# Optimization experiments

Hardware: AMD Instinct MI355X
Metric: run time of the kernel (lower is better)

The kernel has to match this reference:

```python
import jax, jax.numpy as jnp
import numpy as np

S = 3072       # packed sequence length
DIM = 1280     # hidden dim
H = 16         # num heads
HD = DIM // H  # head dim = 80
NEG = -1e9     # additive mask value for cross-segment entries


def setup_inputs() -> dict:
    key = jax.random.key(0)
    ks = jax.random.split(key, 6)
    x = jax.random.normal(ks[0], (S, DIM), jnp.float32)
    # rope angle table [S, HD//2]
    rotary_pos_emb = jax.random.uniform(ks[1], (S, HD // 2), jnp.float32, 0.0, 2.0 * np.pi)
    # 4 equal image segments packed together
    cu_seqlens = jnp.array([0, 768, 1536, 2304, 3072], jnp.int32)
    w_qkv = jax.random.normal(ks[2], (3 * DIM, DIM), jnp.float32) * 0.02
    b_qkv = jax.random.normal(ks[3], (3 * DIM,), jnp.float32) * 0.02
    w_proj = jax.random.normal(ks[4], (DIM, DIM), jnp.float32) * 0.02
    b_proj = jax.random.normal(ks[5], (DIM,), jnp.float32) * 0.02
    return {"x": x, "cu_seqlens": cu_seqlens, "rotary_pos_emb": rotary_pos_emb,
            "w_qkv": w_qkv, "b_qkv": b_qkv, "w_proj": w_proj, "b_proj": b_proj}


def _rope(t, cos, sin):
    # t: [S, H, HD]; cos/sin: [S, 1, HD]
    t1, t2 = jnp.split(t, 2, axis=-1)
    rot = jnp.concatenate([-t2, t1], axis=-1)
    return t * cos + rot * sin


def reference(x, cu_seqlens, rotary_pos_emb, w_qkv, b_qkv, w_proj, b_proj):
    s, d = x.shape
    qkv = (x @ w_qkv.T + b_qkv).reshape(s, 3, H, HD)
    q, k, v = qkv[:, 0], qkv[:, 1], qkv[:, 2]  # each [S, H, HD]

    # NeoX-style rope with tiled (repeated) freqs, computed in fp32
    cos = jnp.cos(rotary_pos_emb)
    sin = jnp.sin(rotary_pos_emb)
    cos = jnp.concatenate([cos, cos], axis=-1)[:, None, :]  # [S,1,HD]
    sin = jnp.concatenate([sin, sin], axis=-1)[:, None, :]
    q = _rope(q.astype(jnp.float32), cos, sin).astype(x.dtype)
    k = _rope(k.astype(jnp.float32), cos, sin).astype(x.dtype)

    # block-diagonal varlen mask from cu_seqlens: segment id per position
    seg = jnp.searchsorted(cu_seqlens, jnp.arange(s), side='right') - 1  # [S]
    mask = jnp.where(seg[:, None] == seg[None, :], 0.0, NEG).astype(x.dtype)  # [S,S]

    scale = 1.0 / np.sqrt(HD).astype(np.float32)
    scores = jnp.einsum('qhd,khd->hqk', q, k) * scale + mask[None]  # [H,S,S]
    attn = jax.nn.softmax(scores, axis=-1)
    out = jnp.einsum('hqk,khd->qhd', attn, v).reshape(s, d)  # [S, DIM]
    return out @ w_proj.T + b_proj
```

## Files before the change

### kernel.cpp

```cpp
#include <hip/hip_runtime.h>


typedef __bf16 bf16;
typedef __bf16 bf16x4 __attribute__((ext_vector_type(4)));
typedef __bf16 bf16x8 __attribute__((ext_vector_type(8)));
typedef float f32x4 __attribute__((ext_vector_type(4)));
typedef float f32x16 __attribute__((ext_vector_type(16)));
typedef unsigned int u32;

constexpr int S = 3072;
constexpr int DIM = 1280;
constexpr int H = 16;
constexpr int HD = 80;
constexpr int KDP = 128;
constexpr int NQKV = 3 * DIM;

constexpr int BM = 192;
constexpr int MB_A = S / BM;
constexpr int NB_B = NQKV / 256;
constexpr int NKT = DIM / 32;
constexpr int ASL = BM * 32 * 2;
constexpr int SLOT = ASL + 16384;

constexpr float QSCALE = 1.4426950408889634f / 8.94427190999916f;

__device__ __forceinline__ void gload_lds16(const void* g, void* l) {
  __builtin_amdgcn_global_load_lds(
      (const __attribute__((address_space(1))) void*)g,
      (__attribute__((address_space(3))) void*)l, 16, 0, 0);
}

__device__ __forceinline__ u32 pkbf2(float a, float b) {
  union { bf16 h[2]; u32 w; } u;
  u.h[0] = (bf16)a; u.h[1] = (bf16)b;
  return u.w;
}

__device__ __forceinline__ int swv(int s) {
  return ((((s >> 3) & 31) ^ ((s & 7) << 2)) << 2);
}

constexpr long PA_CHUNKS = (long)MB_A * NKT * (ASL / 16);
constexpr long PB_CHUNKS = (long)NB_B * NKT * 1024;
constexpr long PW_CHUNKS = (long)DIM * DIM / 8;
constexpr long KP_CHUNKS = (long)H * S * 48 / 8;
constexpr long CS_CHUNKS = (long)S * 40 / 8;
constexpr long TOT_CHUNKS = PA_CHUNKS + PB_CHUNKS + PW_CHUNKS + KP_CHUNKS + CS_CHUNKS;

__global__ __launch_bounds__(256) void pack_inputs(
    const float* __restrict__ x, const float* __restrict__ wq,
    const float* __restrict__ wp, const float* __restrict__ rope,
    bf16* __restrict__ pA, bf16* __restrict__ pB, bf16* __restrict__ wp16,
    bf16* __restrict__ Kb, float* __restrict__ ctab, float* __restrict__ stab) {
  long t = (long)blockIdx.x * 256 + threadIdx.x;
  if (t < PA_CHUNKS) {
    const int blk = (int)(t / (NKT * 768)), rem = (int)(t % (NKT * 768));
    const int kt = rem / 768, c = rem - kt * 768;
    const int lin = c * 16;
    const int logi = lin ^ (((lin >> 7) & 7) << 4);
    const int row = logi >> 6, col = (logi & 63) >> 1;
    const float* src = x + (size_t)(blk * BM + row) * DIM + kt * 32 + col;
    float4 v0 = *(const float4*)src;
    float4 v1 = *(const float4*)(src + 4);
    bf16x8 o = {(bf16)v0.x, (bf16)v0.y, (bf16)v0.z, (bf16)v0.w,
                (bf16)v1.x, (bf16)v1.y, (bf16)v1.z, (bf16)v1.w};
    *(bf16x8*)(pA + t * 8) = o;
  } else if (t < PA_CHUNKS + PB_CHUNKS) {
    long t2 = t - PA_CHUNKS;
    const int blk = (int)(t2 / (NKT * 1024)), rem = (int)(t2 % (NKT * 1024));
    const int kt = rem >> 10, c = rem & 1023;
    const int lin = c * 16;
    const int logi = lin ^ (((lin >> 7) & 7) << 4);
    const int row = logi >> 6, col = (logi & 63) >> 1;
    int grow = blk * 256 + row;
    if (grow < 2560) {
      const int ty = grow / 1280, rm = grow % 1280;
      const int h = rm / 80, p = rm % 80;
      grow = ty * 1280 + h * 80 + (p >> 1) + (p & 1) * 40;
    }
    const float* src = wq + (size_t)grow * DIM + kt * 32 + col;
    float4 v0 = *(const float4*)src;
    float4 v1 = *(const float4*)(src + 4);
    bf16x8 o = {(bf16)v0.x, (bf16)v0.y, (bf16)v0.z, (bf16)v0.w,
                (bf16)v1.x, (bf16)v1.y, (bf16)v1.z, (bf16)v1.w};
    *(bf16x8*)(pB + t2 * 8) = o;
  } else if (t < PA_CHUNKS + PB_CHUNKS + PW_CHUNKS) {
    long t2 = t - PA_CHUNKS - PB_CHUNKS;
    const float* src = wp + t2 * 8;
    float4 v0 = *(const float4*)src;
    float4 v1 = *(const float4*)(src + 4);
    bf16x8 o = {(bf16)v0.x, (bf16)v0.y, (bf16)v0.z, (bf16)v0.w,
                (bf16)v1.x, (bf16)v1.y, (bf16)v1.z, (bf16)v1.w};
    *(bf16x8*)(wp16 + t2 * 8) = o;
  } else if (t < PA_CHUNKS + PB_CHUNKS + PW_CHUNKS + KP_CHUNKS) {
    long t2 = t - PA_CHUNKS - PB_CHUNKS - PW_CHUNKS;
    const int h = (int)(t2 / (S * 6)), r = (int)(t2 % (S * 6));
    const int s = r / 6, cc = r % 6;
    bf16x8 z = {};
    *(bf16x8*)(Kb + ((size_t)h * S + s) * KDP + 80 + cc * 8) = z;
  } else {
    long t3 = t - PA_CHUNKS - PB_CHUNKS - PW_CHUNKS - KP_CHUNKS;
#pragma unroll
    for (int k = 0; k < 8; k++) {
      const int idx = (int)(t3 * 8 + k);
      const int s = idx / 40, a = idx % 40;
      float sn, cs;
      __sincosf(rope[idx], &sn, &cs);
      ctab[a * S + s] = cs;
      stab[a * S + s] = sn;
    }
  }
}

__global__ __launch_bounds__(512, 2) void gemm256(
    const bf16* __restrict__ pA, const bf16* __restrict__ pB,
    const float* __restrict__ bias, const float* __restrict__ ctab,
    const float* __restrict__ stab, bf16* __restrict__ Qb,
    bf16* __restrict__ Kb, bf16* __restrict__ VTb) {
  extern __shared__ char lds[];
  const int tid = threadIdx.x;
  const int w = tid >> 6, lane = tid & 63;
  const int r15 = lane & 15, b4 = lane >> 4;
  const int wr = w >> 2, wc = w & 3;
  const int nwg = gridDim.x * gridDim.y;
  const int orig = blockIdx.y * gridDim.x + blockIdx.x;
  const int xcd = orig % 8, loc = orig / 8;
  const int qq = nwg / 8, rq = nwg % 8;
  const int swzid =
      (xcd < rq ? xcd * (qq + 1) : rq * (qq + 1) + (xcd - rq) * qq) + loc;
  const int nb = swzid % gridDim.x, mb = swzid / gridDim.x;
  const int m0 = mb * BM;
  const char* aPanel = (const char*)pA + (size_t)mb * NKT * ASL;
  const char* bPanel = (const char*)pB + (size_t)nb * NKT * 16384;
  auto stageA = [&](int kt) {
    char* s = lds + (kt & 3) * SLOT;
    const char* g = aPanel + (size_t)kt * ASL;
    gload_lds16(g + tid * 16, s + tid * 16);
    if (tid < 256)
      gload_lds16(g + 8192 + tid * 16, s + 8192 + tid * 16);
  };
  auto stageB = [&](int kt) {
    char* s = lds + (kt & 3) * SLOT + ASL;
    const char* g = bPanel + (size_t)kt * 16384;
    gload_lds16(g + tid * 16, s + tid * 16);
    gload_lds16(g + 8192 + tid * 16, s + 8192 + tid * 16);
  };
  f32x4 acc[6][4] = {};
  stageA(0); stageB(0); stageA(1); stageB(1); stageA(2); stageB(2);
  if (tid < 256) asm volatile("s_waitcnt vmcnt(8)" ::: "memory");
  else           asm volatile("s_waitcnt vmcnt(6)" ::: "memory");
  __builtin_amdgcn_s_barrier();
  for (int kt = 0; kt < NKT; ++kt) {
    const char* As = lds + (kt & 3) * SLOT;
    const char* Bs = As + ASL;
    const bool pf = (kt + 3 < NKT);
    bf16x8 afr[3], bfr[4];
#pragma unroll
    for (int i = 0; i < 3; i++) {
      int a = (wr * 96 + i * 16 + r15) * 64 + b4 * 16;
      a ^= ((a >> 7) & 7) << 4;
      afr[i] = *(const bf16x8*)(As + a);
    }
#pragma unroll
    for (int j = 0; j < 4; j++) {
      int a = (wc * 64 + j * 16 + r15) * 64 + b4 * 16;
      a ^= ((a >> 7) & 7) << 4;
      bfr[j] = *(const bf16x8*)(Bs + a);
    }
    if (pf) stageA(kt + 3);
    asm volatile("" ::: "memory");
    __builtin_amdgcn_s_barrier();
    __builtin_amdgcn_s_setprio(1);
#pragma unroll
    for (int i = 0; i < 3; i++)
#pragma unroll
      for (int j = 0; j < 4; j++)
        acc[i][j] = __builtin_amdgcn_mfma_f32_16x16x32_bf16(afr[i], bfr[j],
                                                            acc[i][j], 0, 0, 0);
    __builtin_amdgcn_s_setprio(0);
    asm volatile("" ::: "memory");
    __builtin_amdgcn_s_barrier();
#pragma unroll
    for (int i = 0; i < 3; i++) {
      int a = (wr * 96 + 48 + i * 16 + r15) * 64 + b4 * 16;
      a ^= ((a >> 7) & 7) << 4;
      afr[i] = *(const bf16x8*)(As + a);
    }
    if (pf) stageB(kt + 3);
    asm volatile("" ::: "memory");
    __builtin_amdgcn_s_barrier();
    __builtin_amdgcn_s_setprio(1);
#pragma unroll
    for (int i = 0; i < 3; i++)
#pragma unroll
      for (int j = 0; j < 4; j++)
        acc[3 + i][j] = __builtin_amdgcn_mfma_f32_16x16x32_bf16(
            afr[i], bfr[j], acc[3 + i][j], 0, 0, 0);
    __builtin_amdgcn_s_setprio(0);
    const int rem = NKT - 2 - kt;
    if (tid < 256) {
      if (rem >= 2)      asm volatile("s_waitcnt vmcnt(8)" ::: "memory");
      else if (rem == 1) asm volatile("s_waitcnt vmcnt(4)" ::: "memory");
      else if (rem == 0) asm volatile("s_waitcnt vmcnt(0)" ::: "memory");
      else               asm volatile("" ::: "memory");
    } else {
      if (rem >= 2)      asm volatile("s_waitcnt vmcnt(6)" ::: "memory");
      else if (rem == 1) asm volatile("s_waitcnt vmcnt(3)" ::: "memory");
      else if (rem == 0) asm volatile("s_waitcnt vmcnt(0)" ::: "memory");
      else               asm volatile("" ::: "memory");
    }
    __builtin_amdgcn_s_barrier();
  }
  const int n0 = nb * 256;
  const int type = n0 / 1280;
  const int cpart0 = n0 - type * 1280;
  if (type < 2) {
#pragma unroll
    for (int j = 0; j < 4; j++) {
      const int c = wc * 64 + j * 16 + r15;
      const int cp = cpart0 + c;
      const int h = cp / 80, p = cp % 80;
      const int d = (p >> 1) + (p & 1) * 40;
      const float bv = bias[type * 1280 + h * 80 + d];
      const int a = p >> 1;
#pragma unroll
      for (int i = 0; i < 6; i++) {
        const int sl = wr * 96 + i * 16 + b4 * 4;
        f32x4 cs4 = *(const f32x4*)&ctab[a * S + m0 + sl];
        f32x4 sn4 = *(const f32x4*)&stab[a * S + m0 + sl];
#pragma unroll
        for (int r = 0; r < 4; r++) {
          float v = acc[i][j][r] + bv;
          float ov = __shfl_xor(v, 1);
          float res = (p & 1) ? (v * cs4[r] + ov * sn4[r])
                              : (v * cs4[r] - ov * sn4[r]);
          if (type == 0) res *= QSCALE;
          *(bf16*)(lds + (sl + r) * 512 + ((2 * c) ^ (((sl + r) & 7) << 4))) =
              (bf16)res;
        }
      }
    }
    __syncthreads();
#pragma unroll
    for (int t = 0; t < 12; t++) {
      const int task = t * 512 + tid;
      const int sl = task >> 5, c = (task & 31) * 8;
      bf16x8 v = *(const bf16x8*)(lds + sl * 512 + ((2 * c) ^ ((sl & 7) << 4)));
      const int cp = cpart0 + c, h = cp / 80, p = cp % 80;
      bf16* dst = type ? Kb + ((size_t)h * S + m0 + sl) * KDP + p
                       : Qb + ((size_t)h * S + m0 + sl) * HD + p;
      *(bf16x8*)dst = v;
    }
  } else {
#pragma unroll
    for (int j = 0; j < 4; j++) {
      const int c = wc * 64 + j * 16 + r15;
      const float bv = bias[2560 + cpart0 + c];
#pragma unroll
      for (int i = 0; i < 6; i++) {
        const int sl = wr * 96 + i * 16 + b4 * 4;
#pragma unroll
        for (int r = 0; r < 4; r++) {
          *(bf16*)(lds + (sl + r) * 512 + ((2 * c) ^ swv(sl + r))) =
              (bf16)(acc[i][j][r] + bv);
        }
      }
    }
    __syncthreads();
#pragma unroll
    for (int t = 0; t < 12; t++) {
      const int task = t * 512 + tid;
      const int c = task & 255, s0 = (task >> 8) * 8;
      union { bf16 h[8]; bf16x8 v; } o;
#pragma unroll
      for (int e = 0; e < 8; e++)
        o.h[e] = *(const bf16*)(lds + (s0 + e) * 512 + ((2 * c) ^ swv(s0 + e)));
      const int cp = cpart0 + c, h = cp / 80, d = cp % 80;
      *(bf16x8*)(VTb + ((size_t)(h * 80 + d)) * S + m0 + s0) = o.v;
    }
  }
}

__global__ __launch_bounds__(256) void gemm_proj(
    const bf16* __restrict__ A, const bf16* __restrict__ B,
    const float* __restrict__ bias, float* __restrict__ Cout, int M, int N,
    int K) {
  __shared__ bf16 Al[2][64 * 32];
  __shared__ bf16 Bl[2][128 * 32];
  const int tid = threadIdx.x;
  const int w = tid >> 6, lane = tid & 63;
  const int r15 = lane & 15, b4 = lane >> 4;
  const int nwg = gridDim.x * gridDim.y;
  const int orig = blockIdx.y * gridDim.x + blockIdx.x;
  const int swzid = (orig & 7) * (nwg >> 3) + (orig >> 3);
  const int bx = swzid % gridDim.x, by = swzid / gridDim.x;
  const int m0 = by * 64, n0 = bx * 128;
  const int wm = (w >> 1) * 32, wn = (w & 1) * 64;
  f32x4 acc[2][4] = {};
  const int row0 = tid >> 2, ko0 = (tid & 3) * 8;
  const bf16* Ar = A + (size_t)(m0 + row0) * K + ko0;
  const bf16* Br0 = B + (size_t)(n0 + row0) * K + ko0;
  const bf16* Br1 = B + (size_t)(n0 + row0 + 64) * K + ko0;

  auto stage = [&](int buf, int k0) {
    gload_lds16(Ar + k0, (char*)Al[buf] + tid * 16);
    gload_lds16(Br0 + k0, (char*)Bl[buf] + tid * 16);
    gload_lds16(Br1 + k0, (char*)Bl[buf] + 4096 + tid * 16);
  };

  stage(0, 0);
  int cur = 0;
  for (int k0 = 0; k0 < K; k0 += 32) {
    __syncthreads();
    if (k0 + 32 < K) stage(cur ^ 1, k0 + 32);
    bf16x8 af[2], bfr[4];
#pragma unroll
    for (int i = 0; i < 2; i++)
      af[i] = *(const bf16x8*)((const char*)Al[cur] + (wm + i * 16 + r15) * 64 + b4 * 16);
#pragma unroll
    for (int j = 0; j < 4; j++)
      bfr[j] = *(const bf16x8*)((const char*)Bl[cur] + (wn + j * 16 + r15) * 64 + b4 * 16);
#pragma unroll
    for (int i = 0; i < 2; i++)
#pragma unroll
      for (int j = 0; j < 4; j++)
        acc[i][j] = __builtin_amdgcn_mfma_f32_16x16x32_bf16(af[i], bfr[j], acc[i][j], 0, 0, 0);
    cur ^= 1;
  }
#pragma unroll
  for (int j = 0; j < 4; j++) {
    const int n = n0 + wn + j * 16 + r15;
    const float bv = bias[n];
#pragma unroll
    for (int i = 0; i < 2; i++) {
      const int mr = m0 + wm + i * 16 + b4 * 4;
#pragma unroll
      for (int r = 0; r < 4; r++)
        Cout[(size_t)(mr + r) * N + n] = acc[i][j][r] + bv;
    }
  }
}

__global__ __launch_bounds__(256, 3) void attn_kern(
    const bf16* __restrict__ Qg, const bf16* __restrict__ Kg,
    const bf16* __restrict__ Vg, const int* __restrict__ cu, int nseg,
    bf16* __restrict__ Out) {
  __shared__ bf16 Kl[2][64 * 128];
  __shared__ bf16 Vl[2][80 * 64];
  const int tid = threadIdx.x, w = tid >> 6, lane = tid & 63;
  const int r31 = lane & 31, hi = lane >> 5;
  const int pair = w >> 1, qs = w & 1;
  const int pt = tid & 127;
  const int nwg = gridDim.x;
  const int orig = blockIdx.x;
  const int swzb = (orig & 7) * (nwg >> 3) + (orig >> 3);
  const int h = swzb / 48, qb = swzb % 48;
  const int q = qb * 64 + qs * 32 + r31;
  int sq = 0, eq = S, lo = 0, hik = S;
  {
    const int qlo = qb * 64, qhi = qb * 64 + 63;
#pragma unroll
    for (int i = 0; i < 8; i++) {
      if (i >= nseg) break;
      int a = cu[i], b = cu[i + 1];
      if (q >= a && q < b) { sq = a; eq = b; }
      if (qlo >= a && qlo < b) lo = a;
      if (qhi >= a && qhi < b) hik = b;
    }
  }
  bf16x8 qf[5];
  {
    const bf16* qrow = Qg + ((size_t)h * S + q) * HD + hi * 8;
#pragma unroll
    for (int kk = 0; kk < 5; kk++) qf[kk] = *(const bf16x8*)(qrow + kk * 16);
  }
  int kdst[8], ksrc[8], vdst[5], vsrc[5];
#pragma unroll
  for (int c = 0; c < 8; c++) {
    int lin = (c * 128 + pt) * 16;
    int row = lin >> 8, colb = (lin & 255) ^ ((row & 15) << 4);
    kdst[c] = lin; ksrc[c] = row * KDP + colb / 2;
  }
#pragma unroll
  for (int c = 0; c < 5; c++) {
    int lin = (c * 128 + pt) * 16;
    int row = lin >> 7, colb = (lin & 127) ^ ((row & 7) << 4);
    vdst[c] = lin; vsrc[c] = row * S + colb / 2;
  }
  const bf16* Kbase = Kg + (size_t)h * S * KDP;
  const bf16* Vbase = Vg + (size_t)h * HD * S;
  char* Klp = (char*)Kl[pair];
  char* Vlp = (char*)Vl[pair];
  auto stage = [&](int k0) {
#pragma unroll
    for (int c = 0; c < 8; c++)
      gload_lds16(Kbase + (size_t)k0 * KDP + ksrc[c], Klp + kdst[c]);
#pragma unroll
    for (int c = 0; c < 5; c++)
      gload_lds16(Vbase + vsrc[c] + k0, Vlp + vdst[c]);
  };
  f32x16 o0 = {}, o1 = {}, o2 = {};
  float m = -1e30f, l = 0.f;
  const int nt = (hik - lo) >> 6;
  const int nit = (nt + 1) >> 1;
  for (int i = 0; i < nit; ++i) {
    const int t = 2 * i + pair;
    const bool act = t < nt;
    const int k0 = lo + t * 64;
    asm volatile("s_waitcnt lgkmcnt(0)" ::: "memory");
    __builtin_amdgcn_s_barrier();
    if (act) stage(k0);
    asm volatile("s_waitcnt vmcnt(5)" ::: "memory");
    __builtin_amdgcn_s_barrier();
    f32x16 st0 = {}, st1 = {};
    float rs = 0.f;
    u32 wd0[4][2], wd1[4][2];
    if (act) {
      __builtin_amdgcn_s_setprio(1);
#pragma unroll
      for (int kk = 0; kk < 5; kk++) {
        const int colb = kk * 32 + hi * 16;
        bf16x8 kf0 = *(const bf16x8*)(Klp + r31 * 256 + (colb ^ ((r31 & 15) << 4)));
        bf16x8 kf1 = *(const bf16x8*)(Klp + (32 + r31) * 256 + (colb ^ ((r31 & 15) << 4)));
        st0 = __builtin_amdgcn_mfma_f32_32x32x16_bf16(kf0, qf[kk], st0, 0, 0, 0);
        st1 = __builtin_amdgcn_mfma_f32_32x32x16_bf16(kf1, qf[kk], st1, 0, 0, 0);
      }
      __builtin_amdgcn_s_setprio(0);
      float tm = -3e38f;
      if (k0 >= sq && k0 + 63 < eq) {
#pragma unroll
        for (int j = 0; j < 16; j++) {
          tm = fmaxf(tm, st0[j]);
          tm = fmaxf(tm, st1[j]);
        }
      } else {
#pragma unroll
        for (int j = 0; j < 16; j++) {
          const int crow = (j & 3) + 8 * (j >> 2) + 4 * hi;
          int key0 = k0 + crow, key1 = k0 + 32 + crow;
          st0[j] = (key0 >= sq && key0 < eq) ? st0[j] : -1e30f;
          st1[j] = (key1 >= sq && key1 < eq) ? st1[j] : -1e30f;
          tm = fmaxf(tm, st0[j]);
          tm = fmaxf(tm, st1[j]);
        }
      }
      tm = fmaxf(tm, __shfl_xor(tm, 32));
      if (!__all(tm <= m + 8.f)) {
        const float mn = fmaxf(m, tm);
        const float alpha = __builtin_amdgcn_exp2f(m - mn);
        o0 *= alpha; o1 *= alpha; o2 *= alpha;
        l *= alpha;
        m = mn;
      }
#pragma unroll
      for (int g2 = 0; g2 < 4; g2++) {
#pragma unroll
        for (int hh = 0; hh < 2; hh++) {
          float a0 = __builtin_amdgcn_exp2f(st0[g2 * 4 + 2 * hh] - m);
          float a1 = __builtin_amdgcn_exp2f(st0[g2 * 4 + 2 * hh + 1] - m);
          float b0 = __builtin_amdgcn_exp2f(st1[g2 * 4 + 2 * hh] - m);
          float b1 = __builtin_amdgcn_exp2f(st1[g2 * 4 + 2 * hh + 1] - m);
          rs += a0 + a1 + b0 + b1;
          wd0[g2][hh] = pkbf2(a0, a1);
          wd1[g2][hh] = pkbf2(b0, b1);
        }
      }
      rs += __shfl_xor(rs, 32);
      l += rs;
    }
    asm volatile("s_waitcnt vmcnt(0)" ::: "memory");
    __builtin_amdgcn_s_barrier();
    if (act) {
      __builtin_amdgcn_s_setprio(1);
#pragma unroll
      for (int kk = 0; kk < 4; kk++) {
        const int g2o = (kk & 1) * 2 + hi;
        const int g2s = (kk & 1) * 2 + (hi ^ 1);
        u32 own0, own1, snd0, snd1;
        if (kk < 2) {
          own0 = wd0[g2o][0]; own1 = wd0[g2o][1];
          snd0 = wd0[g2s][0]; snd1 = wd0[g2s][1];
        } else {
          own0 = wd1[g2o][0]; own1 = wd1[g2o][1];
          snd0 = wd1[g2s][0]; snd1 = wd1[g2s][1];
        }
        u32 rc0 = (u32)__shfl_xor((int)snd0, 32);
        u32 rc1 = (u32)__shfl_xor((int)snd1, 32);
        union { u32 w[4]; bf16x8 v; } pf;
        if (hi == 0) { pf.w[0] = own0; pf.w[1] = own1; pf.w[2] = rc0; pf.w[3] = rc1; }
        else         { pf.w[0] = rc0;  pf.w[1] = rc1;  pf.w[2] = own0; pf.w[3] = own1; }
        const int colb = kk * 32 + hi * 16;
#pragma unroll
        for (int mt = 0; mt < 3; mt++) {
          int row = mt * 32 + r31;
          row = row < HD ? row : 0;
          bf16x8 vf = *(const bf16x8*)(Vlp + row * 128 + (colb ^ ((row & 7) << 4)));
          f32x16* op = mt == 0 ? &o0 : (mt == 1 ? &o1 : &o2);
          *op = __builtin_amdgcn_mfma_f32_32x32x16_bf16(vf, pf.v, *op, 0, 0, 0);
        }
      }
      __builtin_amdgcn_s_setprio(0);
    }
  }
  __syncthreads();
  float* mb = (float*)Kl;
  if (pair == 1) {
    float* d = mb + ((size_t)qs * 64 + lane) * 50;
    d[0] = m; d[1] = l;
#pragma unroll
    for (int j = 0; j < 16; j++) { d[2 + j] = o0[j]; d[18 + j] = o1[j]; d[34 + j] = o2[j]; }
  }
  __syncthreads();
  if (pair == 0) {
    const float* d = mb + ((size_t)qs * 64 + lane) * 50;
    const float pm = d[0], pl = d[1];
    const float mn = fmaxf(m, pm);
    const float a = __builtin_amdgcn_exp2f(m - mn);
    const float b = __builtin_amdgcn_exp2f(pm - mn);
    const float lt = l * a + pl * b;
    const float inv = 1.f / lt;
    bf16* orow = Out + (size_t)q * DIM + h * HD;
#pragma unroll
    for (int rg = 0; rg < 4; rg++) {
      bf16x4 v0, v1;
#pragma unroll
      for (int e = 0; e < 4; e++) {
        v0[e] = (bf16)((o0[rg * 4 + e] * a + d[2 + rg * 4 + e] * b) * inv);
        v1[e] = (bf16)((o1[rg * 4 + e] * a + d[18 + rg * 4 + e] * b) * inv);
      }
      *(bf16x4*)(orow + 8 * rg + 4 * hi) = v0;
      *(bf16x4*)(orow + 32 + 8 * rg + 4 * hi) = v1;
    }
#pragma unroll
    for (int rg = 0; rg < 2; rg++) {
      bf16x4 v2;
#pragma unroll
      for (int e = 0; e < 4; e++)
        v2[e] = (bf16)((o2[rg * 4 + e] * a + d[34 + rg * 4 + e] * b) * inv);
      *(bf16x4*)(orow + 64 + 8 * rg + 4 * hi) = v2;
    }
  }
}

extern "C" void kernel_launch(void* const* d_in, const int* in_sizes, int n_in,
                              void* d_out, int out_size, void* d_ws,
                              size_t ws_size, hipStream_t stream) {
  const float* x = (const float*)d_in[0];
  const int* cu = (const int*)d_in[1];
  const float* rope = (const float*)d_in[2];
  const float* w_qkv = (const float*)d_in[3];
  const float* b_qkv = (const float*)d_in[4];
  const float* w_proj = (const float*)d_in[5];
  const float* b_proj = (const float*)d_in[6];
  const int nseg = in_sizes[1] - 1;

  bf16* pA = (bf16*)d_ws;
  bf16* pB = pA + (size_t)S * DIM;
  bf16* wp16 = pB + (size_t)NQKV * DIM;
  bf16* Qb = wp16 + (size_t)DIM * DIM;
  bf16* Kb = Qb + (size_t)H * S * HD;
  bf16* VTb = Kb + (size_t)H * S * KDP;
  float* ctab = (float*)(VTb + (size_t)H * HD * S);
  float* stab = ctab + (size_t)S * 40;
  bf16* attn16 = pA;

  pack_inputs<<<(int)(TOT_CHUNKS / 256), 256, 0, stream>>>(
      x, w_qkv, w_proj, rope, pA, pB, wp16, Kb, ctab, stab);
  gemm256<<<dim3(NB_B, MB_A), 512, 114688, stream>>>(
      pA, pB, b_qkv, ctab, stab, Qb, Kb, VTb);
  attn_kern<<<H * 48, 256, 0, stream>>>(Qb, Kb, VTb, cu, nseg, attn16);
  gemm_proj<<<dim3(DIM / 128, S / 64), 256, 0, stream>>>(
      attn16, wp16, b_proj, (float*)d_out, S, DIM, DIM);
}
```

Measured before the change: 110.6 us.

## Deepen proj GEMM to 4-stage async pipeline with swizzled LDS layout

New measurement: 106.0 us, median of 2. 4.1% less time.

```diff
diff --git a/kernel.cpp b/kernel.cpp
--- a/kernel.cpp
+++ b/kernel.cpp
@@ -285,47 +285,74 @@
     const bf16* __restrict__ A, const bf16* __restrict__ B,
     const float* __restrict__ bias, float* __restrict__ Cout, int M, int N,
     int K) {
-  __shared__ bf16 Al[2][64 * 32];
-  __shared__ bf16 Bl[2][128 * 32];
+  extern __shared__ char plds[];
   const int tid = threadIdx.x;
   const int w = tid >> 6, lane = tid & 63;
   const int r15 = lane & 15, b4 = lane >> 4;
+  const int wm = (w >> 1) * 32, wn = (w & 1) * 64;
   const int nwg = gridDim.x * gridDim.y;
   const int orig = blockIdx.y * gridDim.x + blockIdx.x;
   const int swzid = (orig & 7) * (nwg >> 3) + (orig >> 3);
   const int bx = swzid % gridDim.x, by = swzid / gridDim.x;
   const int m0 = by * 64, n0 = bx * 128;
-  const int wm = (w >> 1) * 32, wn = (w & 1) * 64;
+  int aR, aC, bR[2], bC[2];
+  {
+    const int lin = tid * 16;
+    const int logi = lin ^ (((lin >> 7) & 7) << 4);
+    aR = logi >> 6; aC = (logi & 63) >> 1;
+  }
+#pragma unroll
+  for (int i = 0; i < 2; i++) {
+    const int lin = tid * 16 + i * 4096;
+    const int logi = lin ^ (((lin >> 7) & 7) << 4);
+    bR[i] = logi >> 6; bC[i] = (logi & 63) >> 1;
+  }
+  const int NT = K / 32;
+  auto stage = [&](int kt) {
+    char* s = plds + (kt & 3) * 12288;
+    gload_lds16(A + (size_t)(m0 + aR) * K + kt * 32 + aC, s + tid * 16);
+#pragma unroll
+    for (int i = 0; i < 2; i++)
+      gload_lds16(B + (size_t)(n0 + bR[i]) * K + kt * 32 + bC[i],
+                  s + 4096 + i * 4096 + tid * 16);
+  };
   f32x4 acc[2][4] = {};
-  const int row0 = tid >> 2, ko0 = (tid & 3) * 8;
-  const bf16* Ar = A + (size_t)(m0 + row0) * K + ko0;
-  const bf16* Br0 = B + (size_t)(n0 + row0) * K + ko0;
-  const bf16* Br1 = B + (size_t)(n0 + row0 + 64) * K + ko0;
-
-  auto stage = [&](int buf, int k0) {
-    gload_lds16(Ar + k0, (char*)Al[buf] + tid * 16);
-    gload_lds16(Br0 + k0, (char*)Bl[buf] + tid * 16);
-    gload_lds16(Br1 + k0, (char*)Bl[buf] + 4096 + tid * 16);
-  };
-
-  stage(0, 0);
-  int cur = 0;
-  for (int k0 = 0; k0 < K; k0 += 32) {
-    __syncthreads();
-    if (k0 + 32 < K) stage(cur ^ 1, k0 + 32);
+  stage(0); stage(1); stage(2);
+  asm volatile("s_waitcnt vmcnt(6)" ::: "memory");
+  __builtin_amdgcn_s_barrier();
+  for (int kt = 0; kt < NT; ++kt) {
+    const char* As = plds + (kt & 3) * 12288;
+    const char* Bs = As + 4096;
     bf16x8 af[2], bfr[4];
 #pragma unroll
+    for (int i = 0; i < 2; i++) {
+      int a = (wm + i * 16 + r15) * 64 + b4 * 16;
+      a ^= ((a >> 7) & 7) << 4;
+      af[i] = *(const bf16x8*)(As + a);
+    }
+#pragma unroll
+    for (int j = 0; j < 4; j++) {
+      int a = (wn + j * 16 + r15) * 64 + b4 * 16;
+      a ^= ((a >> 7) & 7) << 4;
+      bfr[j] = *(const bf16x8*)(Bs + a);
+    }
+    if (kt + 3 < NT) stage(kt + 3);
+    asm volatile("" ::: "memory");
+    __builtin_amdgcn_s_barrier();
+    __builtin_amdgcn_s_setprio(1);
+#pragma unroll
     for (int i = 0; i < 2; i++)
-      af[i] = *(const bf16x8*)((const char*)Al[cur] + (wm + i * 16 + r15) * 64 + b4 * 16);
-#pragma unroll
-    for (int j = 0; j < 4; j++)
-      bfr[j] = *(const bf16x8*)((const char*)Bl[cur] + (wn + j * 16 + r15) * 64 + b4 * 16);
-#pragma unroll
-    for (int i = 0; i < 2; i++)
 #pragma unroll
       for (int j = 0; j < 4; j++)
-        acc[i][j] = __builtin_amdgcn_mfma_f32_16x16x32_bf16(af[i], bfr[j], acc[i][j], 0, 0, 0);
-    cur ^= 1;
+        acc[i][j] = __builtin_amdgcn_mfma_f32_16x16x32_bf16(af[i], bfr[j],
+                                                            acc[i][j], 0, 0, 0);
+    __builtin_amdgcn_s_setprio(0);
+    const int rem = NT - 2 - kt;
+    if (rem >= 2)      asm volatile("s_waitcnt vmcnt(6)" ::: "memory");
+    else if (rem == 1) asm volatile("s_waitcnt vmcnt(3)" ::: "memory");
+    else if (rem == 0) asm volatile("s_waitcnt vmcnt(0)" ::: "memory");
+    else               asm volatile("" ::: "memory");
+    __builtin_amdgcn_s_barrier();
   }
 #pragma unroll
   for (int j = 0; j < 4; j++) {
@@ -569,6 +596,6 @@
   gemm256<<<dim3(NB_B, MB_A), 512, 114688, stream>>>(
       pA, pB, b_qkv, ctab, stab, Qb, Kb, VTb);
   attn_kern<<<H * 48, 256, 0, stream>>>(Qb, Kb, VTb, cu, nseg, attn16);
-  gemm_proj<<<dim3(DIM / 128, S / 64), 256, 0, stream>>>(
+  gemm_proj<<<dim3(DIM / 128, S / 64), 256, 49152, stream>>>(
       attn16, wp16, b_proj, (float*)d_out, S, DIM, DIM);
 }
```
